# Optimization experiments

Measured on AMD Instinct MI355X. Metric: run time of the kernel, lower is better.

## Reference

```python
import jax, jax.numpy as jnp
import numpy as np


def log_g(x):
    # log of g(x) = where(x>=0, x+0.5, sigmoid(x))
    return jnp.where(x >= 0, jnp.log(jax.nn.relu(x) + 0.5), -jax.nn.softplus(-x))


def heinsen_associative_scan_log(log_coeffs, log_values):
    a_star = jnp.cumsum(log_coeffs, axis=1)
    log_h0_plus_b_star = jax.lax.cumlogsumexp(log_values - a_star, axis=1)
    return jnp.exp(a_star + log_h0_plus_b_star)


def setup_inputs() -> dict:
    key = jax.random.key(0)
    k1, k2 = jax.random.split(key)
    B, T, D = 4, 8192, 512
    x = jax.random.normal(k1, (B, T, D), dtype=jnp.float32)
    # Linear(dim, 2*dim, bias=False); scaled like torch default init
    W = jax.random.normal(k2, (D, 2 * D), dtype=jnp.float32) * (1.0 / np.sqrt(D))
    return {"x": x, "W": W}


def reference(x, W):
    hg = jnp.einsum('btd,de->bte', x, W)  # [B,T,2D]
    hidden, gate = jnp.split(hg, 2, axis=-1)
    log_z = -jax.nn.softplus(-gate)       # log sigmoid(gate)
    log_coeffs = -jax.nn.softplus(gate)   # log (1 - sigmoid(gate))
    log_tilde_h = log_g(hidden)
    out = heinsen_associative_scan_log(log_coeffs, log_z + log_tilde_h)
    return out
```

## Files before the change

### kernel.cpp

```cpp
#include <hip/hip_runtime.h>

typedef unsigned short u16;
typedef unsigned int   u32;

typedef __bf16 bf16x8 __attribute__((ext_vector_type(8)));
typedef float  f32x4  __attribute__((ext_vector_type(4)));

#define B_DIM 4
#define T_DIM 8192
#define D_DIM 512
#define M_DIM (B_DIM * T_DIM)
#define K_DIM D_DIM
#define NC    256
#define LCH   32

__device__ __forceinline__ u16 f2bf(float f) {
  u32 u = __float_as_uint(f);
  u32 r = (u + 0x7FFFu + ((u >> 16) & 1u)) >> 16;
  return (u16)r;
}
__device__ __forceinline__ float bf2f(u16 b) {
  return __uint_as_float(((u32)b) << 16);
}

__device__ __forceinline__ void gload_lds16(const u16* g, u16* lds) {
  __builtin_amdgcn_global_load_lds(
      (const __attribute__((address_space(1))) void*)g,
      (__attribute__((address_space(3))) void*)lds, 16, 0, 0);
}


__global__ void convert_x(const float4* __restrict__ in, u16* __restrict__ out, int n4) {
  int i = blockIdx.x * blockDim.x + threadIdx.x;
  int stride = gridDim.x * blockDim.x;
  for (; i < n4; i += stride) {
    float4 f = in[i];
    u32 w0 = (u32)f2bf(f.x) | ((u32)f2bf(f.y) << 16);
    u32 w1 = (u32)f2bf(f.z) | ((u32)f2bf(f.w) << 16);
    *reinterpret_cast<uint2*>(out + (size_t)i * 4) = make_uint2(w0, w1);
  }
}

__global__ void convert_wt(const float* __restrict__ W, u16* __restrict__ wt) {
  int idx = blockIdx.x * blockDim.x + threadIdx.x;
  int n  = idx & 1023;
  int k0 = (idx >> 10) * 8;
  float f[8];
#pragma unroll
  for (int j = 0; j < 8; ++j) f[j] = W[(size_t)(k0 + j) * 1024 + n];
  u32 w[4];
#pragma unroll
  for (int j = 0; j < 4; ++j)
    w[j] = (u32)f2bf(f[2 * j]) | ((u32)f2bf(f[2 * j + 1]) << 16);
  *reinterpret_cast<uint4*>(wt + (size_t)n * 512 + k0) = make_uint4(w[0], w[1], w[2], w[3]);
}


#define BK 32
#define NT 16

__global__ __launch_bounds__(256) void gemm_act(const u16* __restrict__ xb,
                                                const u16* __restrict__ wt,
                                                u32* __restrict__ av_buf,
                                                float* __restrict__ Asum,
                                                float* __restrict__ Bsum) {
  __shared__ u16 As[2][4096];
  __shared__ u16 Bs[2][4096];

  const int tid  = threadIdx.x;
  const int lane = tid & 63;
  const int wave = tid >> 6;
  const int l15  = lane & 15;
  const int lh   = lane >> 4;
  const int wr   = wave >> 1;
  const int wc   = wave & 1;
  const int m_base = blockIdx.x * 128;
  const int d0     = blockIdx.y * 64;

  const int pair0 = tid >> 3;
  const int s3    = (tid & 7) ^ (pair0 & 7);
  const int lrow0 = (pair0 << 1) | (s3 >> 2);
  const int scol  = (s3 & 3) << 3;
  const int garow0 = m_base + lrow0;
  const int garow1 = garow0 + 64;
  const int gn0 = ((lrow0 >> 5) ? 512 : 0) + d0 + (lrow0 & 31);
  const int gn1 = gn0 + 32;
  const int ldsw = wave * 512;

  f32x4 acc[4][4];
#pragma unroll
  for (int m = 0; m < 4; ++m)
#pragma unroll
    for (int n = 0; n < 4; ++n)
      acc[m][n] = (f32x4){0.f, 0.f, 0.f, 0.f};

#define STAGE(buf, kt)                                                      \
  do {                                                                      \
    const int ko = (kt) * BK + scol;                                        \
    gload_lds16(xb + (size_t)garow0 * K_DIM + ko, &As[buf][ldsw]);          \
    gload_lds16(xb + (size_t)garow1 * K_DIM + ko, &As[buf][2048 + ldsw]);   \
    gload_lds16(wt + (size_t)gn0 * K_DIM + ko, &Bs[buf][ldsw]);             \
    gload_lds16(wt + (size_t)gn1 * K_DIM + ko, &Bs[buf][2048 + ldsw]);      \
  } while (0)

#define AOFF(row) (((row) >> 1) * 64 + (((((((row) & 1) << 2) | lh)) ^ (((row) >> 1) & 7)) << 3))

#define COMPUTE(cur)                                                        \
  do {                                                                      \
    bf16x8 af[4], bfr[4];                                                   \
    _Pragma("unroll")                                                       \
    for (int m = 0; m < 4; ++m)                                             \
      af[m] = *reinterpret_cast<const bf16x8*>(&As[cur][AOFF(64 * wr + 16 * m + l15)]); \
    _Pragma("unroll")                                                       \
    for (int n = 0; n < 4; ++n)                                             \
      bfr[n] = *reinterpret_cast<const bf16x8*>(&Bs[cur][AOFF(64 * wc + 16 * n + l15)]); \
    _Pragma("unroll")                                                       \
    for (int m = 0; m < 4; ++m)                                             \
      _Pragma("unroll")                                                     \
      for (int n = 0; n < 4; ++n)                                           \
        acc[m][n] = __builtin_amdgcn_mfma_f32_16x16x32_bf16(af[m], bfr[n], acc[m][n], 0, 0, 0); \
  } while (0)

  STAGE(0, 0);
#pragma unroll
  for (int t = 0; t < NT; t += 2) {
    __syncthreads();
    STAGE(1, t + 1);
    COMPUTE(0);
    __syncthreads();
    if (t + 2 < NT) STAGE(0, t + 2);
    COMPUTE(1);
  }
#undef STAGE
#undef COMPUTE

  const int row_w = m_base + 64 * wr;
#pragma unroll
  for (int h = 0; h < 2; ++h) {
    float Ar[2][2], Br[2][2];
#pragma unroll
    for (int mm = 0; mm < 2; ++mm) {
      const int m = 2 * h + mm;
#pragma unroll
      for (int n = 0; n < 2; ++n) {
        float A = 1.f, Bv = 0.f;
        const int dch = d0 + 32 * wc + 16 * n + l15;
#pragma unroll
        for (int r = 0; r < 4; ++r) {
          float hid = acc[m][n][r];
          float gt  = acc[m][n + 2][r];
          float e   = __expf(gt);
          float inv = 1.f / (1.f + e);
          float g   = (hid >= 0.f) ? (hid + 0.5f) : (1.f / (1.f + __expf(-hid)));
          float v   = (e * inv) * g;
          u16 abf = f2bf(inv);
          u16 vbf = f2bf(v);
          const int grow = row_w + 16 * m + 4 * lh + r;
          av_buf[(size_t)grow * D_DIM + dch] = (u32)abf | ((u32)vbf << 16);
          float af = bf2f(abf), vf = bf2f(vbf);
          Bv = af * Bv + vf;
          A *= af;
        }
        Ar[n][mm] = A; Br[n][mm] = Bv;
      }
    }
#pragma unroll
    for (int n = 0; n < 2; ++n)
#pragma unroll
      for (int mm = 0; mm < 2; ++mm) {
        float A = Ar[n][mm], Bv = Br[n][mm];
#pragma unroll
        for (int d = 1; d <= 2; d <<= 1) {
          float pA = __shfl(A, lane - 16 * d);
          float pB = __shfl(Bv, lane - 16 * d);
          if (lh >= d) { Bv = A * pB + Bv; A = A * pA; }
        }
        Ar[n][mm] = A; Br[n][mm] = Bv;
      }
    if (lh == 3) {
      const int grow = row_w + 32 * h;
      const int b = grow >> 13;
      const int c = (grow & 8191) >> 5;
      const size_t o = ((size_t)(b * NC + c)) * D_DIM;
#pragma unroll
      for (int n = 0; n < 2; ++n) {
        const int dch = d0 + 32 * wc + 16 * n + l15;
        float Ac = Ar[n][0] * Ar[n][1];
        float Bc = Ar[n][1] * Br[n][0] + Br[n][1];
        Asum[o + dch] = Ac;
        Bsum[o + dch] = Bc;
      }
    }
  }
}


__global__ __launch_bounds__(256) void scan_pass2(const float* __restrict__ Asum,
                                                  const float* __restrict__ Bsum,
                                                  float* __restrict__ carry) {
  int idx = blockIdx.x * blockDim.x + threadIdx.x;
  int b = idx >> 9;
  int d = idx & 511;
  float h = 0.f;
  for (int c = 0; c < NC; ++c) {
    size_t o = ((size_t)(b * NC + c)) * D_DIM + d;
    carry[o] = h;
    h = Asum[o] * h + Bsum[o];
  }
}


__global__ __launch_bounds__(128) void scan_pass3(const u32* __restrict__ av_buf,
                                                  const float4* __restrict__ carry,
                                                  float4* __restrict__ out) {
  const int c = blockIdx.x;
  const int b = blockIdx.y;
  const int d4 = threadIdx.x;
  float4 hh = carry[((size_t)(b * NC + c)) * 128 + d4];
  float h[4] = {hh.x, hh.y, hh.z, hh.w};
  size_t base = ((size_t)b * T_DIM + (size_t)c * LCH) * D_DIM + d4 * 4;
  for (int t = 0; t < LCH; ++t) {
    uint4 w = *reinterpret_cast<const uint4*>(av_buf + base);
    h[0] = bf2f(w.x & 0xffff) * h[0] + bf2f(w.x >> 16);
    h[1] = bf2f(w.y & 0xffff) * h[1] + bf2f(w.y >> 16);
    h[2] = bf2f(w.z & 0xffff) * h[2] + bf2f(w.z >> 16);
    h[3] = bf2f(w.w & 0xffff) * h[3] + bf2f(w.w >> 16);
    out[base >> 2] = make_float4(h[0], h[1], h[2], h[3]);
    base += D_DIM;
  }
}


extern "C" void kernel_launch(void* const* d_in, const int* in_sizes, int n_in,
                              void* d_out, int out_size, void* d_ws, size_t ws_size,
                              hipStream_t stream) {
  const float* x = (const float*)d_in[0];
  const float* W = (const float*)d_in[1];
  float* out = (float*)d_out;

  char* ws = (char*)d_ws;
  u16*   xb     = (u16*)(ws + 0);
  u16*   wtp    = (u16*)(ws + 33554432);
  u32*   av_buf = (u32*)(ws + 34603008);
  float* Asum   = (float*)(ws + 101711872);
  float* Bsum   = (float*)(ws + 103809024);
  float* carry  = (float*)(ws + 105906176);
  if (ws_size < 108003328ULL) return;

  convert_x<<<2048, 256, 0, stream>>>((const float4*)x, xb, (M_DIM * K_DIM) / 4);
  convert_wt<<<256, 256, 0, stream>>>(W, wtp);
  gemm_act<<<dim3(M_DIM / 128, D_DIM / 64), 256, 0, stream>>>(xb, wtp, av_buf, Asum, Bsum);
  scan_pass2<<<8, 256, 0, stream>>>(Asum, Bsum, carry);
  scan_pass3<<<dim3(NC, B_DIM), 128, 0, stream>>>(av_buf, (const float4*)carry, (float4*)out);
}
```

Before: 120.6 us.

## Enlarge GEMM tile to 256 rows with 8 waves and triple-buffered LDS pipeline

Result: faster. 114.5 us (-5.1%).

```diff
diff --git a/kernel.cpp b/kernel.cpp
--- a/kernel.cpp
+++ b/kernel.cpp
@@ -59,13 +59,13 @@
 #define BK 32
 #define NT 16
 
-__global__ __launch_bounds__(256) void gemm_act(const u16* __restrict__ xb,
-                                                const u16* __restrict__ wt,
-                                                u32* __restrict__ av_buf,
-                                                float* __restrict__ Asum,
-                                                float* __restrict__ Bsum) {
-  __shared__ u16 As[2][4096];
-  __shared__ u16 Bs[2][4096];
+__global__ __launch_bounds__(512, 4) void gemm_act(const u16* __restrict__ xb,
+                                                   const u16* __restrict__ wt,
+                                                   u32* __restrict__ av_buf,
+                                                   float* __restrict__ Asum,
+                                                   float* __restrict__ Bsum) {
+  __shared__ u16 As[3][8192];
+  __shared__ u16 Bs[3][4096];
 
   const int tid  = threadIdx.x;
   const int lane = tid & 63;
@@ -74,17 +74,17 @@
   const int lh   = lane >> 4;
   const int wr   = wave >> 1;
   const int wc   = wave & 1;
-  const int m_base = blockIdx.x * 128;
+  const int m_base = blockIdx.x * 256;
   const int d0     = blockIdx.y * 64;
 
-  const int pair0 = tid >> 3;
-  const int s3    = (tid & 7) ^ (pair0 & 7);
-  const int lrow0 = (pair0 << 1) | (s3 >> 2);
-  const int scol  = (s3 & 3) << 3;
-  const int garow0 = m_base + lrow0;
-  const int garow1 = garow0 + 64;
-  const int gn0 = ((lrow0 >> 5) ? 512 : 0) + d0 + (lrow0 & 31);
-  const int gn1 = gn0 + 32;
+  const int pairl = tid >> 3;
+  const int slog  = (tid & 7) ^ (pairl & 7);
+  const int lrow  = (pairl << 1) | (slog >> 2);
+  const int scol  = (slog & 3) << 3;
+  const int garow0 = m_base + lrow;
+  const int garow1 = garow0 + 128;
+  const int pB = lrow >> 5;
+  const int gn = ((pB & 1) ? 512 : 0) + d0 + ((pB >> 1) << 5) + (lrow & 31);
   const int ldsw = wave * 512;
 
   f32x4 acc[4][4];
@@ -98,9 +98,8 @@
   do {                                                                      \
     const int ko = (kt) * BK + scol;                                        \
     gload_lds16(xb + (size_t)garow0 * K_DIM + ko, &As[buf][ldsw]);          \
-    gload_lds16(xb + (size_t)garow1 * K_DIM + ko, &As[buf][2048 + ldsw]);   \
-    gload_lds16(wt + (size_t)gn0 * K_DIM + ko, &Bs[buf][ldsw]);             \
-    gload_lds16(wt + (size_t)gn1 * K_DIM + ko, &Bs[buf][2048 + ldsw]);      \
+    gload_lds16(xb + (size_t)garow1 * K_DIM + ko, &As[buf][4096 + ldsw]);   \
+    gload_lds16(wt + (size_t)gn * K_DIM + ko, &Bs[buf][ldsw]);              \
   } while (0)
 
 #define AOFF(row) (((row) >> 1) * 64 + (((((((row) & 1) << 2) | lh)) ^ (((row) >> 1) & 7)) << 3))
@@ -121,18 +120,24 @@
         acc[m][n] = __builtin_amdgcn_mfma_f32_16x16x32_bf16(af[m], bfr[n], acc[m][n], 0, 0, 0); \
   } while (0)
 
+#define WAITV(N) asm volatile("s_waitcnt vmcnt(" #N ")" ::: "memory")
+#define BAR()    asm volatile("s_barrier" ::: "memory")
+
   STAGE(0, 0);
-#pragma unroll
-  for (int t = 0; t < NT; t += 2) {
-    __syncthreads();
-    STAGE(1, t + 1);
-    COMPUTE(0);
-    __syncthreads();
-    if (t + 2 < NT) STAGE(0, t + 2);
-    COMPUTE(1);
-  }
+  STAGE(1, 1);
+#pragma unroll
+  for (int t = 0; t < 14; ++t) {
+    WAITV(3);
+    BAR();
+    STAGE((t + 2) % 3, t + 2);
+    COMPUTE(t % 3);
+  }
+  WAITV(3); BAR(); COMPUTE(2);
+  WAITV(0); BAR(); COMPUTE(0);
 #undef STAGE
 #undef COMPUTE
+#undef WAITV
+#undef BAR
 
   const int row_w = m_base + 64 * wr;
 #pragma unroll
@@ -249,7 +254,7 @@
 
   convert_x<<<2048, 256, 0, stream>>>((const float4*)x, xb, (M_DIM * K_DIM) / 4);
   convert_wt<<<256, 256, 0, stream>>>(W, wtp);
-  gemm_act<<<dim3(M_DIM / 128, D_DIM / 64), 256, 0, stream>>>(xb, wtp, av_buf, Asum, Bsum);
+  gemm_act<<<dim3(M_DIM / 256, 8), 512, 0, stream>>>(xb, wtp, av_buf, Asum, Bsum);
   scan_pass2<<<8, 256, 0, stream>>>(Asum, Bsum, carry);
   scan_pass3<<<dim3(NC, B_DIM), 128, 0, stream>>>(av_buf, (const float4*)carry, (float4*)out);
 }
```
